# Performance work log

Measured on AMD Instinct MI355X. Metric: run time of the kernel, lower is better.

The kernel has to match this reference:

```python
import jax, jax.numpy as jnp
import numpy as np

EMB = 1024
HEADS = 16
HEAD_DIM = EMB // HEADS
EPS = 1e-5


def gelu_tanh(x):
    c = jnp.sqrt(jnp.asarray(2.0 / jnp.pi, x.dtype))
    return 0.5 * x * (1 + jnp.tanh(c * (x + 0.044715 * x ** 3)))


def layernorm(x, scale, shift):
    mean = jnp.mean(x, axis=-1, keepdims=True)
    var = jnp.mean((x - mean) ** 2, axis=-1, keepdims=True)
    return scale * (x - mean) / jnp.sqrt(var + EPS) + shift


def setup_inputs() -> dict:
    key = jax.random.key(0)
    ks = jax.random.split(key, 12)
    s = 0.02
    x = jax.random.normal(ks[0], (2, 2048, EMB), dtype=jnp.float32)
    Wq = jax.random.normal(ks[1], (EMB, EMB), dtype=jnp.float32) * s
    Wk = jax.random.normal(ks[2], (EMB, EMB), dtype=jnp.float32) * s
    Wv = jax.random.normal(ks[3], (EMB, EMB), dtype=jnp.float32) * s
    Wo = jax.random.normal(ks[4], (EMB, EMB), dtype=jnp.float32) * s
    bo = jnp.zeros((EMB,), jnp.float32)
    W1 = jax.random.normal(ks[5], (EMB, 4 * EMB), dtype=jnp.float32) * s
    b1 = jnp.zeros((4 * EMB,), jnp.float32)
    W2 = jax.random.normal(ks[6], (4 * EMB, EMB), dtype=jnp.float32) * s
    b2 = jnp.zeros((EMB,), jnp.float32)
    g1 = jnp.ones((EMB,), jnp.float32)
    s1 = jnp.zeros((EMB,), jnp.float32)
    g2 = jnp.ones((EMB,), jnp.float32)
    s2 = jnp.zeros((EMB,), jnp.float32)
    return {"x": x, "Wq": Wq, "Wk": Wk, "Wv": Wv, "Wo": Wo, "bo": bo,
            "W1": W1, "b1": b1, "W2": W2, "b2": b2,
            "g1": g1, "s1": s1, "g2": g2, "s2": s2}


def reference(x, Wq, Wk, Wv, Wo, bo, W1, b1, W2, b2, g1, s1, g2, s2):
    B, S, D = x.shape
    # --- attention sub-block (pre-LN) ---
    h = layernorm(x, g1, s1)
    q = (h @ Wq).reshape(B, S, HEADS, HEAD_DIM).transpose(0, 2, 1, 3)
    k = (h @ Wk).reshape(B, S, HEADS, HEAD_DIM).transpose(0, 2, 1, 3)
    v = (h @ Wv).reshape(B, S, HEADS, HEAD_DIM).transpose(0, 2, 1, 3)
    scores = jnp.einsum('bhqd,bhkd->bhqk', q, k) / jnp.sqrt(
        jnp.asarray(HEAD_DIM, x.dtype))
    causal = jnp.triu(jnp.ones((S, S), bool), k=1)
    scores = jnp.where(causal, -jnp.inf, scores)
    attn = jax.nn.softmax(scores, axis=-1)
    ctx = jnp.einsum('bhqk,bhkd->bhqd', attn, v)
    ctx = ctx.transpose(0, 2, 1, 3).reshape(B, S, D)
    x = x + (ctx @ Wo + bo)
    # --- FFN sub-block (pre-LN) ---
    h = layernorm(x, g2, s2)
    h = gelu_tanh(h @ W1 + b1) @ W2 + b2
    return x + h
```

## Files before the change

### kernel.cpp

```cpp
#include <hip/hip_runtime.h>
#include <hip/hip_bf16.h>
#include <math.h>
#include <stdint.h>

typedef __bf16 bf16;
typedef __bf16 bf16x4 __attribute__((ext_vector_type(4)));
typedef __bf16 bf16x8 __attribute__((ext_vector_type(8)));
typedef float f32x4 __attribute__((ext_vector_type(4)));

#define MFMA16(a, b, c) __builtin_amdgcn_mfma_f32_16x16x32_bf16((a), (b), (c), 0, 0, 0)

constexpr int EMB = 1024;
constexpr int SEQ = 2048;
constexpr int BATCH = 2;
constexpr int NTOK = BATCH * SEQ;
constexpr int FFN = 4 * EMB;
constexpr int HEADS = 16;
constexpr int HDIM = 64;

#define QSCALE 0.18033688011112042f

__device__ __forceinline__ void gload16(const void* g, void* l) {
    __builtin_amdgcn_global_load_lds(
        (const __attribute__((address_space(1))) void*)g,
        (__attribute__((address_space(3))) void*)l,
        16, 0, 0);
}

__global__ __launch_bounds__(256) void ln_kernel(const float* __restrict__ x,
                                                 const float* __restrict__ g,
                                                 const float* __restrict__ b,
                                                 bf16* __restrict__ out) {
    int row = blockIdx.x;
    int t = threadIdx.x;
    float4 v = reinterpret_cast<const float4*>(x + (size_t)row * EMB)[t];
    float s = v.x + v.y + v.z + v.w;
    float s2 = v.x * v.x + v.y * v.y + v.z * v.z + v.w * v.w;
#pragma unroll
    for (int o = 1; o < 64; o <<= 1) {
        s += __shfl_xor(s, o);
        s2 += __shfl_xor(s2, o);
    }
    __shared__ float ps[4], ps2[4];
    int w = t >> 6;
    if ((t & 63) == 0) { ps[w] = s; ps2[w] = s2; }
    __syncthreads();
    s = ps[0] + ps[1] + ps[2] + ps[3];
    s2 = ps2[0] + ps2[1] + ps2[2] + ps2[3];
    float mean = s * (1.f / EMB);
    float var = s2 * (1.f / EMB) - mean * mean;
    float rstd = rsqrtf(var + 1e-5f);
    float4 gv = reinterpret_cast<const float4*>(g)[t];
    float4 bv = reinterpret_cast<const float4*>(b)[t];
    bf16* op = out + (size_t)row * EMB + t * 4;
    op[0] = (bf16)(gv.x * (v.x - mean) * rstd + bv.x);
    op[1] = (bf16)(gv.y * (v.y - mean) * rstd + bv.y);
    op[2] = (bf16)(gv.z * (v.z - mean) * rstd + bv.z);
    op[3] = (bf16)(gv.w * (v.w - mean) * rstd + bv.w);
}

__global__ __launch_bounds__(256) void transpose_all(
    const float* __restrict__ Wq, const float* __restrict__ Wk,
    const float* __restrict__ Wv, const float* __restrict__ Wo,
    const float* __restrict__ W1, const float* __restrict__ W2,
    bf16* __restrict__ Wqkvt, bf16* __restrict__ Wot,
    bf16* __restrict__ W1t, bf16* __restrict__ W2t) {
    int b = blockIdx.x;
    const float* W;
    bf16* Wt;
    int K, N, tile;
    if (b < 4096) {
        int w = b >> 10;
        tile = b & 1023;
        W = (w == 0) ? Wq : (w == 1) ? Wk : (w == 2) ? Wv : Wo;
        Wt = (w == 3) ? Wot : Wqkvt + (size_t)w * EMB * EMB;
        K = EMB; N = EMB;
    } else if (b < 8192) {
        tile = b - 4096; W = W1; Wt = W1t; K = EMB; N = FFN;
    } else {
        tile = b - 8192; W = W2; Wt = W2t; K = FFN; N = EMB;
    }
    int ntx = N / 32;
    int n0 = (tile % ntx) * 32, k0 = (tile / ntx) * 32;
    __shared__ float tl[32][33];
    int tx = threadIdx.x & 31, ty = threadIdx.x >> 5;
#pragma unroll
    for (int i = 0; i < 4; i++)
        tl[ty + 8 * i][tx] = W[(size_t)(k0 + ty + 8 * i) * N + n0 + tx];
    __syncthreads();
#pragma unroll
    for (int i = 0; i < 4; i++)
        Wt[(size_t)(n0 + ty + 8 * i) * K + k0 + tx] = (bf16)tl[tx][ty + 8 * i];
}

__global__ __launch_bounds__(256) void vtrans(const bf16* __restrict__ v,
                                              bf16* __restrict__ vt) {
    int bh = blockIdx.y;
    int s0 = blockIdx.x * 64;
    const bf16* src = v + (size_t)bh * SEQ * HDIM + (size_t)s0 * HDIM;
    bf16* dst = vt + (size_t)bh * HDIM * SEQ + s0;
    __shared__ bf16 tile[64][72];
    int t = threadIdx.x;
    int s = t >> 2, d0 = (t & 3) * 16;
    bf16x8 a = *reinterpret_cast<const bf16x8*>(src + s * HDIM + d0);
    bf16x8 b = *reinterpret_cast<const bf16x8*>(src + s * HDIM + d0 + 8);
#pragma unroll
    for (int e = 0; e < 8; e++) {
        tile[d0 + e][s] = a[e];
        tile[d0 + 8 + e][s] = b[e];
    }
    __syncthreads();
    int d = t >> 2, c0 = (t & 3) * 16;
    bf16x8 o0 = *reinterpret_cast<const bf16x8*>(&tile[d][c0]);
    bf16x8 o1 = *reinterpret_cast<const bf16x8*>(&tile[d][c0 + 8]);
    *reinterpret_cast<bf16x8*>(dst + (size_t)d * SEQ + c0) = o0;
    *reinterpret_cast<bf16x8*>(dst + (size_t)d * SEQ + c0 + 8) = o1;
}

template <int MODE>
__global__ __launch_bounds__(512, 1) void gemm8p(const bf16* __restrict__ A,
                                                 const bf16* __restrict__ Bt,
                                                 int K, int N,
                                                 bf16* __restrict__ outB,
                                                 const float* __restrict__ bias) {
    extern __shared__ char smem[];
    int t = threadIdx.x;
    int wave = t >> 6, lane = t & 63;
    int wr = wave >> 2, wc = wave & 3;
    int lr = lane & 15, lg = lane >> 4;
    int row0 = blockIdx.x * 256;
    int col0 = blockIdx.y * 256;

    const char* aSrc[4];
    const char* bSrc[4];
#pragma unroll
    for (int i = 0; i < 4; i++) {
        int f = t + i * 512;
        int gr = f >> 3, gk = f & 7;
        aSrc[i] = (const char*)A + ((size_t)(row0 + gr) * K + ((gk ^ (gr & 7)) << 3)) * 2;
        bSrc[i] = (const char*)Bt + ((size_t)(col0 + gr) * K + ((gk ^ (gr & 7)) << 3)) * 2;
    }

    f32x4 acc[8][4];
#pragma unroll
    for (int m = 0; m < 8; m++)
#pragma unroll
        for (int n = 0; n < 4; n++) acc[m][n] = f32x4{0.f, 0.f, 0.f, 0.f};

#pragma unroll
    for (int i = 0; i < 4; i++) {
        gload16(aSrc[i], smem + (t + i * 512) * 16);
        gload16(bSrc[i], smem + 32768 + (t + i * 512) * 16);
    }
    __syncthreads();

    int nt = K / 64;
    for (int tk = 0; tk < nt; tk++) {
        int cur = tk & 1;
        const char* la = smem + cur * 65536;
        const char* lb = la + 32768;
        char* na = smem + (cur ^ 1) * 65536;
        bool stage = (tk + 1 < nt);

        bf16x8 bfr[2][4];
#pragma unroll
        for (int ph = 0; ph < 4; ph++) {
            constexpr int PH_KH[4] = {0, 0, 1, 1};
            constexpr int PH_MH[4] = {0, 1, 0, 1};
            const int kh = PH_KH[ph], mh = PH_MH[ph];
            bf16x8 afr[4];
#pragma unroll
            for (int m = 0; m < 4; m++) {
                int row = wr * 128 + (mh * 4 + m) * 16 + lr;
                int gk = kh * 4 + lg;
                afr[m] = *reinterpret_cast<const bf16x8*>(
                    la + row * 128 + ((gk ^ (row & 7)) << 4));
            }
            if (mh == 0) {
#pragma unroll
                for (int n = 0; n < 4; n++) {
                    int row = wc * 64 + n * 16 + lr;
                    int gk = kh * 4 + lg;
                    bfr[kh][n] = *reinterpret_cast<const bf16x8*>(
                        lb + row * 128 + ((gk ^ (row & 7)) << 4));
                }
            }
            if (stage) {
                gload16(aSrc[ph] + 128, na + (t + ph * 512) * 16);
                gload16(bSrc[ph] + 128, na + 32768 + (t + ph * 512) * 16);
            }
            __builtin_amdgcn_s_barrier();
            __builtin_amdgcn_s_setprio(1);
#pragma unroll
            for (int m = 0; m < 4; m++)
#pragma unroll
                for (int n = 0; n < 4; n++)
                    acc[mh * 4 + m][n] = MFMA16(afr[m], bfr[kh][n], acc[mh * 4 + m][n]);
            __builtin_amdgcn_s_setprio(0);
            __builtin_amdgcn_s_barrier();
        }
#pragma unroll
        for (int i = 0; i < 4; i++) { aSrc[i] += 128; bSrc[i] += 128; }
        __syncthreads();
    }

    float bi[4];
    if (MODE == 2) {
#pragma unroll
        for (int n = 0; n < 4; n++) bi[n] = bias[col0 + wc * 64 + n * 16 + lr];
    }
#pragma unroll
    for (int mf = 0; mf < 8; mf++) {
#pragma unroll
        for (int r = 0; r < 4; r++) {
            int row = row0 + wr * 128 + mf * 16 + 4 * lg + r;
#pragma unroll
            for (int n = 0; n < 4; n++) {
                int col = col0 + wc * 64 + n * 16 + lr;
                float v = acc[mf][n][r];
                if (MODE == 0) {
                    int b_ = row >> 11, s_ = row & 2047;
                    int which = col >> 10, rem = col & 1023;
                    int h_ = rem >> 6, d_ = rem & 63;
                    float sc = (which == 0) ? QSCALE : 1.0f;
                    outB[(size_t)which * (NTOK * EMB) +
                         (((size_t)(b_ * HEADS + h_) * SEQ + s_) << 6) + d_] =
                        (bf16)(v * sc);
                } else {
                    float u = v + bi[n];
                    float gl = 0.5f * u *
                               (1.f + tanhf(0.7978845608028654f *
                                            (u + 0.044715f * u * u * u)));
                    outB[(size_t)row * N + col] = (bf16)gl;
                }
            }
        }
    }
}

template <int BM, int BN, int BK, int MODE>
__global__ __launch_bounds__(256) void gemm_lds(const bf16* __restrict__ A,
                                                const bf16* __restrict__ Bt,
                                                int M, int N, int K,
                                                float* __restrict__ outF,
                                                bf16* __restrict__ outB,
                                                const float* __restrict__ bias,
                                                const float* __restrict__ resid) {
    constexpr int MR = BM / 32;
    constexpr int NR = BN / 32;
    constexpr int ACH = (BM * BK * 2) / 4096;
    constexpr int BCH = (BN * BK * 2) / 4096;
    __shared__ bf16 sA[BM * BK];
    __shared__ bf16 sB[BN * BK];
    int t = threadIdx.x;
    int wave = t >> 6, lane = t & 63;
    int wr = wave >> 1, wc = wave & 1;
    int lr = lane & 15, lg = lane >> 4;
    int row0 = blockIdx.x * BM;
    int col0 = blockIdx.y * BN;

    const char* aS[ACH];
    const char* bS[BCH];
#pragma unroll
    for (int c = 0; c < ACH; c++) {
        int o = (t + c * 256) * 16;
        aS[c] = (const char*)A + (size_t)(row0 + o / (2 * BK)) * K * 2 + (o & (2 * BK - 1));
    }
#pragma unroll
    for (int c = 0; c < BCH; c++) {
        int o = (t + c * 256) * 16;
        bS[c] = (const char*)Bt + (size_t)(col0 + o / (2 * BK)) * K * 2 + (o & (2 * BK - 1));
    }

    f32x4 acc[MR][NR];
#pragma unroll
    for (int m = 0; m < MR; m++)
#pragma unroll
        for (int n = 0; n < NR; n++) acc[m][n] = f32x4{0.f, 0.f, 0.f, 0.f};

    for (int k0 = 0; k0 < K; k0 += BK) {
        __syncthreads();
#pragma unroll
        for (int c = 0; c < ACH; c++)
            gload16(aS[c], (char*)sA + (t + c * 256) * 16);
#pragma unroll
        for (int c = 0; c < BCH; c++)
            gload16(bS[c], (char*)sB + (t + c * 256) * 16);
#pragma unroll
        for (int c = 0; c < ACH; c++) aS[c] += 2 * BK;
#pragma unroll
        for (int c = 0; c < BCH; c++) bS[c] += 2 * BK;
        __syncthreads();

#pragma unroll
        for (int ks = 0; ks < BK / 32; ks++) {
            bf16x8 a[MR], b[NR];
#pragma unroll
            for (int m = 0; m < MR; m++)
                a[m] = *reinterpret_cast<const bf16x8*>(
                    sA + (wr * (BM / 2) + m * 16 + lr) * BK + ks * 32 + 8 * lg);
#pragma unroll
            for (int n = 0; n < NR; n++)
                b[n] = *reinterpret_cast<const bf16x8*>(
                    sB + (wc * (BN / 2) + n * 16 + lr) * BK + ks * 32 + 8 * lg);
#pragma unroll
            for (int m = 0; m < MR; m++)
#pragma unroll
                for (int n = 0; n < NR; n++)
                    acc[m][n] = MFMA16(a[m], b[n], acc[m][n]);
        }
    }

#pragma unroll
    for (int m = 0; m < MR; m++) {
#pragma unroll
        for (int r = 0; r < 4; r++) {
            int row = row0 + wr * (BM / 2) + m * 16 + 4 * lg + r;
#pragma unroll
            for (int n = 0; n < NR; n++) {
                int col = col0 + wc * (BN / 2) + n * 16 + lr;
                float v = acc[m][n][r];
                size_t idx = (size_t)row * N + col;
                outF[idx] = resid[idx] + v + bias[col];
            }
        }
    }
}

__global__ __launch_bounds__(256, 3) void attn_kernel(const bf16* __restrict__ q,
                                                      const bf16* __restrict__ k,
                                                      const bf16* __restrict__ vt,
                                                      bf16* __restrict__ ctx) {
    int wg = blockIdx.x;
    int wgid = (wg & 7) * 64 + (wg >> 3);
    int bh = wgid >> 4;
    int pair = wgid & 15;
    const bf16* qh = q + (size_t)bh * SEQ * HDIM;
    const bf16* kh = k + (size_t)bh * SEQ * HDIM;
    const bf16* vh = vt + (size_t)bh * HDIM * SEQ;
    int t = threadIdx.x;
    int wave = t >> 6, lane = t & 63;
    int lr = lane & 15, lg = lane >> 4;

    __shared__ bf16 sK[2][64 * 64];
    __shared__ bf16 sV[2][64 * 64];
    __shared__ bf16 plds[4][16][88];

    int grow = t >> 3, gg = t & 7;
    const bf16* kSrc0 = kh + (size_t)grow * HDIM + ((gg ^ (grow & 7)) << 3);
    const bf16* kSrc1 = kh + (size_t)(grow + 32) * HDIM + ((gg ^ ((grow + 32) & 7)) << 3);
    const bf16* vSrc0 = vh + (size_t)grow * SEQ + ((gg ^ (grow & 7)) << 3);
    const bf16* vSrc1 = vh + (size_t)(grow + 32) * SEQ + ((gg ^ ((grow + 32) & 7)) << 3);
    char* kD0 = (char*)&sK[0][0] + wave * 1024;
    char* vD0 = (char*)&sV[0][0] + wave * 1024;

    int swz = (lr & 7) << 4;
    int koff0 = (16 * lg) ^ swz;
    int koff1 = (64 + 16 * lg) ^ swz;
    int b_ = bh >> 4, h_ = bh & 15;

    for (int seg = 0; seg < 2; seg++) {
        int q0 = (seg == 0 ? (31 - pair) : pair) * 64;
        int qrow = q0 + wave * 16;

        bf16x8 qf0 = *reinterpret_cast<const bf16x8*>(
            qh + (size_t)(qrow + lr) * HDIM + 8 * lg);
        bf16x8 qf1 = *reinterpret_cast<const bf16x8*>(
            qh + (size_t)(qrow + lr) * HDIM + 32 + 8 * lg);

        f32x4 o[4];
#pragma unroll
        for (int n = 0; n < 4; n++) o[n] = f32x4{0.f, 0.f, 0.f, 0.f};
        float mx[4] = {-1e30f, -1e30f, -1e30f, -1e30f};
        float lsum[4] = {0.f, 0.f, 0.f, 0.f};

        int nc = q0 / 64 + 1;

        gload16(kSrc0, kD0);
        gload16(kSrc1, kD0 + 4096);
        gload16(vSrc0, vD0);
        gload16(vSrc1, vD0 + 4096);
        __syncthreads();

        for (int c = 0; c < nc; c++) {
            int c0 = c * 64;
            if (c + 1 < nc) {
                int nb = (c + 1) & 1;
                int cn = c0 + 64;
                gload16(kSrc0 + (size_t)cn * HDIM, kD0 + nb * 8192);
                gload16(kSrc1 + (size_t)cn * HDIM, kD0 + nb * 8192 + 4096);
                gload16(vSrc0 + cn, vD0 + nb * 8192);
                gload16(vSrc1 + cn, vD0 + nb * 8192 + 4096);
            }
            const char* kb_ = (const char*)&sK[c & 1][0];
            const char* vb_ = (const char*)&sV[c & 1][0];

            f32x4 st[4];
#pragma unroll
            for (int n = 0; n < 4; n++) {
                int ro = (16 * n + lr) * 128;
                bf16x8 kf0 = *reinterpret_cast<const bf16x8*>(kb_ + ro + koff0);
                bf16x8 kf1 = *reinterpret_cast<const bf16x8*>(kb_ + ro + koff1);
                f32x4 a = f32x4{0.f, 0.f, 0.f, 0.f};
                a = MFMA16(qf0, kf0, a);
                a = MFMA16(qf1, kf1, a);
                st[n] = a;
            }

            if (c0 == q0) {
#pragma unroll
                for (int n = 0; n < 4; n++)
#pragma unroll
                    for (int r = 0; r < 4; r++)
                        if (c0 + n * 16 + lr > qrow + 4 * lg + r) st[n][r] = -1e30f;
            }

            float mn[4], scl[4], ps[4];
#pragma unroll
            for (int r = 0; r < 4; r++) {
                float mp = fmaxf(fmaxf(st[0][r], st[1][r]), fmaxf(st[2][r], st[3][r]));
#pragma unroll
                for (int off = 1; off < 16; off <<= 1)
                    mp = fmaxf(mp, __shfl_xor(mp, off));
                mn[r] = fmaxf(mx[r], mp);
                scl[r] = __builtin_amdgcn_exp2f(mx[r] - mn[r]);
                mx[r] = mn[r];
                ps[r] = 0.f;
            }
#pragma unroll
            for (int n = 0; n < 4; n++)
#pragma unroll
                for (int r = 0; r < 4; r++) {
                    float p = __builtin_amdgcn_exp2f(st[n][r] - mn[r]);
                    ps[r] += p;
                    plds[wave][4 * lg + r][n * 16 + lr] = (bf16)p;
                }
#pragma unroll
            for (int r = 0; r < 4; r++) {
                float s = ps[r];
#pragma unroll
                for (int off = 1; off < 16; off <<= 1) s += __shfl_xor(s, off);
                lsum[r] = lsum[r] * scl[r] + s;
            }
#pragma unroll
            for (int n = 0; n < 4; n++) {
                o[n][0] *= scl[0]; o[n][1] *= scl[1];
                o[n][2] *= scl[2]; o[n][3] *= scl[3];
            }

#pragma unroll
            for (int ks = 0; ks < 2; ks++) {
                bf16x8 pa = *reinterpret_cast<const bf16x8*>(
                    &plds[wave][lr][ks * 32 + 8 * lg]);
                int vo = (64 * ks + 16 * lg) ^ swz;
#pragma unroll
                for (int n = 0; n < 4; n++) {
                    bf16x8 vf = *reinterpret_cast<const bf16x8*>(
                        vb_ + (16 * n + lr) * 128 + vo);
                    o[n] = MFMA16(pa, vf, o[n]);
                }
            }

            __syncthreads();
        }

#pragma unroll
        for (int r = 0; r < 4; r++) {
            float inv = 1.f / lsum[r];
            size_t base = ((size_t)b_ * SEQ + qrow + 4 * lg + r) * EMB + h_ * HDIM;
#pragma unroll
            for (int n = 0; n < 4; n++)
                ctx[base + n * 16 + lr] = (bf16)(o[n][r] * inv);
        }
    }
}

extern "C" void kernel_launch(void* const* d_in, const int* in_sizes, int n_in,
                              void* d_out, int out_size, void* d_ws, size_t ws_size,
                              hipStream_t stream) {
    const float* x  = (const float*)d_in[0];
    const float* Wq = (const float*)d_in[1];
    const float* Wk = (const float*)d_in[2];
    const float* Wv = (const float*)d_in[3];
    const float* Wo = (const float*)d_in[4];
    const float* bo = (const float*)d_in[5];
    const float* W1 = (const float*)d_in[6];
    const float* b1 = (const float*)d_in[7];
    const float* W2 = (const float*)d_in[8];
    const float* b2 = (const float*)d_in[9];
    const float* g1 = (const float*)d_in[10];
    const float* s1 = (const float*)d_in[11];
    const float* g2 = (const float*)d_in[12];
    const float* s2 = (const float*)d_in[13];

    const size_t MB = 1ull << 20;
    char* w = (char*)d_ws;
    bf16* Wqkvt = (bf16*)(w + 0 * MB);
    bf16* Wot = (bf16*)(w + 6 * MB);
    bf16* W1t = (bf16*)(w + 8 * MB);
    bf16* W2t = (bf16*)(w + 16 * MB);
    bf16* hbuf = (bf16*)(w + 24 * MB);
    bf16* vtb  = (bf16*)(w + 24 * MB);
    bf16* qkvb = (bf16*)(w + 32 * MB);
    bf16* qb   = (bf16*)(w + 32 * MB);
    bf16* kb   = (bf16*)(w + 40 * MB);
    bf16* vb   = (bf16*)(w + 48 * MB);
    bf16* ctxb = (bf16*)(w + 56 * MB);
    bf16* midb = (bf16*)(w + 32 * MB);
    float* x1  = (float*)(w + 64 * MB);

    hipFuncSetAttribute(reinterpret_cast<const void*>(gemm8p<0>),
                        hipFuncAttributeMaxDynamicSharedMemorySize, 131072);
    hipFuncSetAttribute(reinterpret_cast<const void*>(gemm8p<2>),
                        hipFuncAttributeMaxDynamicSharedMemorySize, 131072);

    transpose_all<<<dim3(12288), 256, 0, stream>>>(Wq, Wk, Wv, Wo, W1, W2,
                                                   Wqkvt, Wot, W1t, W2t);

    ln_kernel<<<NTOK, 256, 0, stream>>>(x, g1, s1, hbuf);

    gemm8p<0><<<dim3(NTOK / 256, 3072 / 256), 512, 131072, stream>>>(
        hbuf, Wqkvt, EMB, 3072, qkvb, nullptr);

    vtrans<<<dim3(SEQ / 64, BATCH * HEADS), 256, 0, stream>>>(vb, vtb);

    attn_kernel<<<dim3(512), 256, 0, stream>>>(qb, kb, vtb, ctxb);

    gemm_lds<128, 64, 32, 1><<<dim3(NTOK / 128, EMB / 64), 256, 0, stream>>>(
        ctxb, Wot, NTOK, EMB, EMB, x1, nullptr, bo, x);

    ln_kernel<<<NTOK, 256, 0, stream>>>(x1, g2, s2, hbuf);

    gemm8p<2><<<dim3(NTOK / 256, FFN / 256), 512, 131072, stream>>>(
        hbuf, W1t, EMB, FFN, midb, b1);

    gemm_lds<128, 64, 32, 1><<<dim3(NTOK / 128, EMB / 64), 256, 0, stream>>>(
        midb, W2t, NTOK, EMB, FFN, (float*)d_out, nullptr, b2, x1);
}
```

Before: 276.6 us.

## Move FFN down-projection to split-K gemm8p with separate bias/residual reduction

The second FFN GEMM (K=4096) now runs on the large 256x256 gemm8p kernel instead of the smaller gemm_lds kernel. K is split three ways over blockIdx.z so that 64 output tiles become 192 blocks. Each slice writes bf16 partial sums into reused workspace regions. A new elementwise kernel then adds the three partials, the bias and the fp32 residual. This trades the less efficient tile kernel for an extra partial-sum write and read pass, and rounds the partials to bf16, which loses some precision.

```diff
diff --git a/kernel.cpp b/kernel.cpp
--- a/kernel.cpp
+++ b/kernel.cpp
@@ -122,6 +122,7 @@
                                                  const bf16* __restrict__ Bt,
                                                  int K, int N,
                                                  bf16* __restrict__ outB,
+                                                 bf16* __restrict__ outB2,
                                                  const float* __restrict__ bias) {
     extern __shared__ char smem[];
     int t = threadIdx.x;
@@ -131,14 +132,22 @@
     int row0 = blockIdx.x * 256;
     int col0 = blockIdx.y * 256;
 
+    int tilesAll = K / 64;
+    int nz = gridDim.z, z = blockIdx.z;
+    int base = tilesAll / nz, rem = tilesAll - base * nz;
+    int myT = base + (z < rem ? 1 : 0);
+    int tBeg = z * base + (z < rem ? z : rem);
+
     const char* aSrc[4];
     const char* bSrc[4];
 #pragma unroll
     for (int i = 0; i < 4; i++) {
         int f = t + i * 512;
         int gr = f >> 3, gk = f & 7;
-        aSrc[i] = (const char*)A + ((size_t)(row0 + gr) * K + ((gk ^ (gr & 7)) << 3)) * 2;
-        bSrc[i] = (const char*)Bt + ((size_t)(col0 + gr) * K + ((gk ^ (gr & 7)) << 3)) * 2;
+        aSrc[i] = (const char*)A + ((size_t)(row0 + gr) * K + ((gk ^ (gr & 7)) << 3)) * 2
+                  + (size_t)tBeg * 128;
+        bSrc[i] = (const char*)Bt + ((size_t)(col0 + gr) * K + ((gk ^ (gr & 7)) << 3)) * 2
+                  + (size_t)tBeg * 128;
     }
 
     f32x4 acc[8][4];
@@ -154,13 +163,12 @@
     }
     __syncthreads();
 
-    int nt = K / 64;
-    for (int tk = 0; tk < nt; tk++) {
+    for (int tk = 0; tk < myT; tk++) {
         int cur = tk & 1;
         const char* la = smem + cur * 65536;
         const char* lb = la + 32768;
         char* na = smem + (cur ^ 1) * 65536;
-        bool stage = (tk + 1 < nt);
+        bool stage = (tk + 1 < myT);
 
         bf16x8 bfr[2][4];
 #pragma unroll
@@ -209,6 +217,8 @@
 #pragma unroll
         for (int n = 0; n < 4; n++) bi[n] = bias[col0 + wc * 64 + n * 16 + lr];
     }
+    bf16* pd = outB;
+    if (MODE == 3) pd = (z < 2) ? outB + (size_t)z * ((size_t)NTOK * EMB) : outB2;
 #pragma unroll
     for (int mf = 0; mf < 8; mf++) {
 #pragma unroll
@@ -220,21 +230,44 @@
                 float v = acc[mf][n][r];
                 if (MODE == 0) {
                     int b_ = row >> 11, s_ = row & 2047;
-                    int which = col >> 10, rem = col & 1023;
-                    int h_ = rem >> 6, d_ = rem & 63;
+                    int which = col >> 10, rem_ = col & 1023;
+                    int h_ = rem_ >> 6, d_ = rem_ & 63;
                     float sc = (which == 0) ? QSCALE : 1.0f;
                     outB[(size_t)which * (NTOK * EMB) +
                          (((size_t)(b_ * HEADS + h_) * SEQ + s_) << 6) + d_] =
                         (bf16)(v * sc);
-                } else {
+                } else if (MODE == 2) {
                     float u = v + bi[n];
                     float gl = 0.5f * u *
                                (1.f + tanhf(0.7978845608028654f *
                                             (u + 0.044715f * u * u * u)));
                     outB[(size_t)row * N + col] = (bf16)gl;
+                } else {
+                    pd[(size_t)row * N + col] = (bf16)v;
                 }
             }
         }
+    }
+}
+
+__global__ __launch_bounds__(256) void ffn2_reduce(const float* __restrict__ x1,
+                                                   const bf16* __restrict__ p01,
+                                                   const bf16* __restrict__ p2,
+                                                   const float* __restrict__ bias,
+                                                   float* __restrict__ out) {
+    constexpr int UNITS = NTOK * EMB / 4;
+    const bf16* p1 = p01 + (size_t)NTOK * EMB;
+    for (int i = blockIdx.x * 256 + threadIdx.x; i < UNITS; i += gridDim.x * 256) {
+        float4 r = reinterpret_cast<const float4*>(x1)[i];
+        float4 bv = reinterpret_cast<const float4*>(bias)[i & (EMB / 4 - 1)];
+        bf16x4 a0 = reinterpret_cast<const bf16x4*>(p01)[i];
+        bf16x4 a1 = reinterpret_cast<const bf16x4*>(p1)[i];
+        bf16x4 a2 = reinterpret_cast<const bf16x4*>(p2)[i];
+        r.x += (float)a0[0] + (float)a1[0] + (float)a2[0] + bv.x;
+        r.y += (float)a0[1] + (float)a1[1] + (float)a2[1] + bv.y;
+        r.z += (float)a0[2] + (float)a1[2] + (float)a2[2] + bv.z;
+        r.w += (float)a0[3] + (float)a1[3] + (float)a2[3] + bv.w;
+        reinterpret_cast<float4*>(out)[i] = r;
     }
 }
 
@@ -508,11 +541,15 @@
     bf16* ctxb = (bf16*)(w + 56 * MB);
     bf16* midb = (bf16*)(w + 32 * MB);
     float* x1  = (float*)(w + 64 * MB);
+    bf16* p01  = (bf16*)(w + 0 * MB);
+    bf16* p2   = (bf16*)(w + 24 * MB);
 
     hipFuncSetAttribute(reinterpret_cast<const void*>(gemm8p<0>),
                         hipFuncAttributeMaxDynamicSharedMemorySize, 131072);
     hipFuncSetAttribute(reinterpret_cast<const void*>(gemm8p<2>),
                         hipFuncAttributeMaxDynamicSharedMemorySize, 131072);
+    hipFuncSetAttribute(reinterpret_cast<const void*>(gemm8p<3>),
+                        hipFuncAttributeMaxDynamicSharedMemorySize, 131072);
 
     transpose_all<<<dim3(12288), 256, 0, stream>>>(Wq, Wk, Wv, Wo, W1, W2,
                                                    Wqkvt, Wot, W1t, W2t);
@@ -520,7 +557,7 @@
     ln_kernel<<<NTOK, 256, 0, stream>>>(x, g1, s1, hbuf);
 
     gemm8p<0><<<dim3(NTOK / 256, 3072 / 256), 512, 131072, stream>>>(
-        hbuf, Wqkvt, EMB, 3072, qkvb, nullptr);
+        hbuf, Wqkvt, EMB, 3072, qkvb, nullptr, nullptr);
 
     vtrans<<<dim3(SEQ / 64, BATCH * HEADS), 256, 0, stream>>>(vb, vtb);
 
@@ -532,8 +569,9 @@
     ln_kernel<<<NTOK, 256, 0, stream>>>(x1, g2, s2, hbuf);
 
     gemm8p<2><<<dim3(NTOK / 256, FFN / 256), 512, 131072, stream>>>(
-        hbuf, W1t, EMB, FFN, midb, b1);
-
-    gemm_lds<128, 64, 32, 1><<<dim3(NTOK / 128, EMB / 64), 256, 0, stream>>>(
-        midb, W2t, NTOK, EMB, FFN, (float*)d_out, nullptr, b2, x1);
-}
+        hbuf, W1t, EMB, FFN, midb, nullptr, b1);
+
+    gemm8p<3><<<dim3(NTOK / 256, EMB / 256, 3), 512, 131072, stream>>>(
+        midb, W2t, FFN, EMB, p01, p2, nullptr);
+    ffn2_reduce<<<dim3(2048), 256, 0, stream>>>(x1, p01, p2, b2, (float*)d_out);
+}
```

New measurement: 255.5 us. 1.08x faster.
